# Kernel tuning notes

Measured on AMD Instinct MI355X. Metric: run time of the kernel, lower is better.

The kernel has to match this reference:

```python
import jax, jax.numpy as jnp
import numpy as np

L_FREQ = 6            # positional-encoding frequencies -> enc dim 3 + 3*2*6 = 39
SKIP = 4              # skip-connection layer index
BMIN, BMAX = -1.0, 1.0
RESCALE = 1.0
SCALE_MLP = 1.0
SDF_THR = 5e-5
ITERS_MAX = 8
RES = 128             # opt.Res (MAX_SAMPLES)
B, R = 1, 8192
N = B * R
PICK = 4096


def embed(xyz):
    # rescale into the AABB then NeRF positional encoding; (..., 3) -> (..., 39)
    xn = ((xyz - BMIN) / (BMAX - BMIN) * 2.0 - 1.0) * RESCALE
    freqs = (2.0 ** jnp.arange(L_FREQ)).astype(xyz.dtype)
    ang = xn[..., None, :] * freqs[:, None]                # (..., L, 3)
    flat = ang.reshape(*ang.shape[:-2], -1)                # (..., 3*L)
    return jnp.concatenate([xn, jnp.sin(flat), jnp.cos(flat)], axis=-1)


def mlp(enc, ws, bs):
    # VolSDF Geometry MLP: softplus(beta=100) activations, skip concat at layer SKIP
    h = enc
    for i in range(len(ws)):
        if i == SKIP:
            h = jnp.concatenate([h, enc], axis=-1)
        h = h @ ws[i] + bs[i]
        if i < len(ws) - 1:
            h = jax.nn.softplus(100.0 * h) / 100.0
    return h


def infer_sdf(xyz, ws, bs):
    # opt.data.inside == True, bg_sdf == False branch
    return mlp(embed(xyz), ws, bs)[..., 0] / SCALE_MLP


def ray_aabb(o, d):
    # slab test (RayAABBIntersector): entry/exit distances, near clamped to 0
    inv = 1.0 / d
    t1 = (BMIN - o) * inv
    t2 = (BMAX - o) * inv
    tmin = jnp.max(jnp.minimum(t1, t2), axis=-1)
    tmax = jnp.min(jnp.maximum(t1, t2), axis=-1)
    return jnp.maximum(tmin, 0.0), tmax


def sphere_trace(o, d, ws, bs):
    # o, d: (N, 3). Runs exactly ITERS_MAX masked iterations (the torch loop only
    # breaks early when ALL rays converge; masked rays add curr_sdf==0 so the
    # per-ray math is identical).
    tmin, tmax = ray_aabb(o, d)
    p_s = o + tmin[:, None] * d
    next_s = infer_sdf(p_s, ws, bs)
    next_e = infer_sdf(o + tmax[:, None] * d, ws, bs)
    mask_s = jnp.ones((o.shape[0],), bool)
    mask_e = jnp.ones((o.shape[0],), bool)

    def step(carry, _):
        acc_s, acc_e, next_s, next_e, mask_s, mask_e, p_s = carry
        curr_s = jnp.where(jnp.abs(next_s) <= SDF_THR, 0.0, next_s)
        curr_e = jnp.where(jnp.abs(next_e) <= SDF_THR, 0.0, next_e)
        mask_s = mask_s & (jnp.abs(curr_s) > SDF_THR)
        mask_e = mask_e & (jnp.abs(curr_e) > SDF_THR)
        track_pt = p_s                                  # appended BEFORE the march
        acc_s = jnp.minimum(acc_s + curr_s, tmax)
        acc_e = jnp.minimum(acc_e + curr_e, tmax)
        p_s = o + acc_s[:, None] * d
        p_e = o + acc_e[:, None] * d
        next_s = jnp.where(mask_s, infer_sdf(p_s, ws, bs), next_s)
        next_e = jnp.where(mask_e, infer_sdf(p_e, ws, bs), next_e)
        ok = acc_s < acc_e
        return (acc_s, acc_e, next_s, next_e, mask_s & ok, mask_e & ok, p_s), track_pt

    carry0 = (tmin, tmax, next_s, next_e, mask_s, mask_e, p_s)
    carry, track = jax.lax.scan(step, carry0, None, length=ITERS_MAX)
    acc_e = carry[1]
    pts_tracks = jnp.transpose(track, (1, 0, 2))        # (N, T, 3)
    return pts_tracks, acc_e, tmin, tmax


def setup_inputs() -> dict:
    key = jax.random.key(0)
    ks = jax.random.split(key, 16)
    u = jax.random.normal(ks[0], (B, R, 3), jnp.float32)
    u = u / jnp.linalg.norm(u, axis=-1, keepdims=True)
    ray0 = 3.0 * u                                       # origins on radius-3 sphere
    tgt = 0.3 * jax.random.normal(ks[1], (B, R, 3), jnp.float32)
    rd = tgt - ray0
    ray_direction = rd / jnp.linalg.norm(rd, axis=-1, keepdims=True)
    factor_rand = jax.random.uniform(ks[2], (B, R), jnp.float32)
    pick_ind = jax.random.permutation(ks[3], N)[:PICK].astype(jnp.int32)
    dims_in = [39, 256, 256, 256, 295, 256, 256, 256, 256]
    dims_out = [256] * 8 + [257]
    inp = {"ray0": ray0, "ray_direction": ray_direction,
           "factor_rand": factor_rand, "pick_ind": pick_ind}
    for i in range(9):
        inp[f"w{i}"] = jax.random.normal(ks[4 + (i % 12)], (dims_in[i], dims_out[i]),
                                           jnp.float32) / np.sqrt(dims_in[i]).astype(np.float32)
        inp[f"b{i}"] = jnp.zeros((dims_out[i],), jnp.float32)
    return inp


def reference(ray0, ray_direction, factor_rand, pick_ind,
              w0, b0, w1, b1, w2, b2, w3, b3, w4, b4, w5, b5, w6, b6, w7, b7, w8, b8):
    ws = [w0, w1, w2, w3, w4, w5, w6, w7, w8]
    bs = [b0, b1, b2, b3, b4, b5, b6, b7, b8]
    o = ray0.reshape(-1, 3)
    d = ray_direction.reshape(-1, 3)
    pts_tracks, acc_e, min_dis, max_dis = sphere_trace(o, d, ws, bs)
    sdf_tracks = infer_sdf(pts_tracks, ws, bs)          # (N, T)
    sdf_sum = jnp.sum(sdf_tracks, axis=-1)              # (N,)
    shp = ray0.shape[:-1]
    d_pred = jnp.minimum((sdf_sum + min_dis).reshape(shp), max_dis.reshape(shp))
    finish_mask = jnp.abs(sdf_tracks[:, -1]) < (BMAX - BMIN) / 10.0 / RES
    d_up = jnp.minimum(1.5 * acc_e.reshape(shp), max_dis.reshape(shp))
    d_sample = (1.0 - factor_rand) * d_up + factor_rand * min_dis.reshape(shp)
    sampled = ray0 + d_sample[..., None] * ray_direction
    sampled_pts = jnp.concatenate([pts_tracks[pick_ind].reshape(1, -1, 3),
                                   sampled.reshape(1, -1, 3)], axis=1)
    return d_pred, sdf_tracks[:, -1], sampled_pts, finish_mask
```

## Files before the change

### kernel.cpp

```cpp
#include <hip/hip_runtime.h>
#include <math.h>

#define NR 8192
#define NPICK 4096
#define SDF_THR_C 5e-5f

#define OUT_DPRED 0
#define OUT_SDFL  8192
#define OUT_SAMP  16384
#define OUT_FIN   139264

typedef __attribute__((ext_vector_type(8))) short short8v;
typedef __attribute__((ext_vector_type(4))) float f32x4;

#define SK  320
#define SKB 640

struct Wptrs { const float* w[8]; };
struct EvalP {
  const float* b[8];
  const float* b8;
  const unsigned short* WTi;
  const float* w8c;
};

__device__ __forceinline__ unsigned short f2bf(float f) {
  unsigned int u = __float_as_uint(f);
  unsigned int r = u + 0x7FFFu + ((u >> 16) & 1u);
  return (unsigned short)(r >> 16);
}
__device__ __forceinline__ float bf2f(unsigned short h) {
  return __uint_as_float(((unsigned int)h) << 16);
}
__device__ __forceinline__ float softplus100(float h) {
  float z = 100.0f * h;
  return (fmaxf(z, 0.0f) + __logf(1.0f + __expf(-fabsf(z)))) * 0.01f;
}

__global__ void prep_transpose(Wptrs wp, unsigned short* __restrict__ WTi)
{
  __shared__ unsigned short sh[64 * 66];
  __shared__ unsigned short sl[64 * 66];
  const int Kreal[8] = {39,256,256,256,295,256,256,256};
  const int Kp[8]    = {64,256,256,256,320,256,256,256};
  const int WB[8]    = {0,16384,81920,147456,212992,294912,360448,425984};
  const int cum[9]   = {0,4,20,36,52,72,88,104,120};
  int b = blockIdx.x;
  int l = 0;
  while (l < 7 && b >= cum[l + 1]) ++l;
  int tile = b - cum[l];
  int tk_n = Kp[l] >> 6;
  int tk = tile % tk_n, tc = tile / tk_n;
  const float* __restrict__ W = wp.w[l];
  int t = threadIdx.x;
  #pragma unroll
  for (int i = 0; i < 16; ++i) {
    int id = t + i * 256;
    int kl = id >> 6, cl = id & 63;
    int k = tk * 64 + kl, c = tc * 64 + cl;
    float v = (k < Kreal[l]) ? W[k * 256 + c] : 0.0f;
    unsigned short h = f2bf(v);
    unsigned short lo = f2bf(v - bf2f(h));
    sh[kl * 66 + cl] = h;
    sl[kl * 66 + cl] = lo;
  }
  __syncthreads();
  const int nksL = Kp[l] >> 5;
  #pragma unroll
  for (int i = 0; i < 16; ++i) {
    int id = t + i * 256;
    int cl = id >> 6, kl = id & 63;
    int col = tc * 64 + cl;
    int k = tk * 64 + kl;
    int g = col >> 4, lr = col & 15;
    int ksg = k >> 5, lq = (k >> 3) & 3, e = k & 7;
    int lane = lq * 16 + lr;
    size_t base = 2 * (size_t)WB[l] + ((size_t)(g * nksL + ksg)) * 1024 + lane * 8 + e;
    WTi[base]       = sh[kl * 66 + cl];
    WTi[base + 512] = sl[kl * 66 + cl];
  }
}

__global__ void prep_w8(const float* __restrict__ w8, float* __restrict__ w8c)
{
  int t = threadIdx.x;
  w8c[t] = w8[(size_t)t * 257];
}

template<int NKS, int KPL>
__device__ __forceinline__ void layer_bpre(
    const unsigned short* __restrict__ wt, const float* __restrict__ bias,
    unsigned short* Ah, unsigned short* Al,
    int lq, int lr, int cw, int swA)
{
  const char* ahc = (const char*)Ah;
  const char* alc = (const char*)Al;
  f32x4 acc[4];
  #pragma unroll
  for (int i = 0; i < 4; ++i) acc[i] = (f32x4){0.f, 0.f, 0.f, 0.f};

  const int col = cw + lr;
  const unsigned short* wcol = wt + (size_t)(cw >> 4) * NKS * 1024 + (lq * 16 + lr) * 8;

  short8v Bh[2], Bl[2];
  Bh[0] = *(const short8v*)(wcol);
  Bl[0] = *(const short8v*)(wcol + 512);

  #pragma unroll
  for (int ks = 0; ks < NKS; ++ks) {
    const int cur = ks & 1, nxt = cur ^ 1;
    if (ks + 1 < NKS) {
      const unsigned short* wn = wcol + (size_t)(ks + 1) * 1024;
      Bh[nxt] = *(const short8v*)(wn);
      Bl[nxt] = *(const short8v*)(wn + 512);
    }
    int ax = (ks * 64 + lq * 16) ^ swA;
    short8v ah[4], al[4];
    #pragma unroll
    for (int rt = 0; rt < 4; ++rt) {
      ah[rt] = *(const short8v*)(ahc + (rt * 16 + lr) * SKB + ax);
      al[rt] = *(const short8v*)(alc + (rt * 16 + lr) * SKB + ax);
    }
    #pragma unroll
    for (int rt = 0; rt < 4; ++rt) {
      acc[rt] = __builtin_amdgcn_mfma_f32_16x16x32_bf16(ah[rt], Bh[cur], acc[rt], 0, 0, 0);
      acc[rt] = __builtin_amdgcn_mfma_f32_16x16x32_bf16(al[rt], Bh[cur], acc[rt], 0, 0, 0);
      acc[rt] = __builtin_amdgcn_mfma_f32_16x16x32_bf16(ah[rt], Bl[cur], acc[rt], 0, 0, 0);
    }
  }

  __syncthreads();

  char* ahw = (char*)Ah;
  char* alw = (char*)Al;
  {
    float bv = bias[col];
    int cb2 = col * 2;
    #pragma unroll
    for (int rt = 0; rt < 4; ++rt) {
      #pragma unroll
      for (int r = 0; r < 4; ++r) {
        float h = softplus100(acc[rt][r] + bv);
        unsigned short hh = f2bf(h);
        unsigned short hl = f2bf(h - bf2f(hh));
        int row = rt * 16 + lq * 4 + r;
        int addr = row * SKB + (cb2 ^ ((row & 7) << 4));
        *(unsigned short*)(ahw + addr) = hh;
        *(unsigned short*)(alw + addr) = hl;
      }
    }
  }
  __syncthreads();
}

__global__ __launch_bounds__(1024, 1)
void eval_mfma(const float* __restrict__ pts, float* __restrict__ sdf_out, EvalP P)
{
  __shared__ __align__(16) unsigned short Ah[64 * SK];
  __shared__ __align__(16) unsigned short Al[64 * SK];
  __shared__ float enc[64 * 40];
  __shared__ float red[8 * 64];
  const int WBA[8] = {0,16384,81920,147456,212992,294912,360448,425984};

  const int t = threadIdx.x;
  const int rbase = blockIdx.x * 64;

  if (t < 64) {
    const int r = rbase + t;
    float x = pts[3*r+0], y = pts[3*r+1], z = pts[3*r+2];
    float xn = ((x + 1.0f) * 0.5f) * 2.0f - 1.0f;
    float yn = ((y + 1.0f) * 0.5f) * 2.0f - 1.0f;
    float zn = ((z + 1.0f) * 0.5f) * 2.0f - 1.0f;
    float* row = enc + t * 40;
    row[0] = xn; row[1] = yn; row[2] = zn;
    float f = 1.0f;
    for (int lf = 0; lf < 6; ++lf) {
      float ax = xn * f, ay = yn * f, az = zn * f;
      row[3  + lf*3 + 0] = sinf(ax);
      row[3  + lf*3 + 1] = sinf(ay);
      row[3  + lf*3 + 2] = sinf(az);
      row[21 + lf*3 + 0] = cosf(ax);
      row[21 + lf*3 + 1] = cosf(ay);
      row[21 + lf*3 + 2] = cosf(az);
      f *= 2.0f;
    }
  }
  __syncthreads();

  {
    char* ahp = (char*)Ah;
    char* alp = (char*)Al;
    int row = t >> 4, c4 = t & 15;
    int sw = (row & 7) << 4;
    #pragma unroll
    for (int reg = 0; reg < 2; ++reg) {
      int koff = reg ? 256 : 0;
      #pragma unroll
      for (int e = 0; e < 4; e += 2) {
        int kl = c4 * 4 + e;
        float v0 = (kl     < 39) ? enc[row * 40 + kl]     : 0.0f;
        float v1 = (kl + 1 < 39) ? enc[row * 40 + kl + 1] : 0.0f;
        unsigned short h0 = f2bf(v0), h1 = f2bf(v1);
        unsigned short q0 = f2bf(v0 - bf2f(h0)), q1 = f2bf(v1 - bf2f(h1));
        int addr = row * SKB + (((koff + kl) * 2) ^ sw);
        *(unsigned int*)(ahp + addr) = (unsigned)h0 | ((unsigned)h1 << 16);
        *(unsigned int*)(alp + addr) = (unsigned)q0 | ((unsigned)q1 << 16);
      }
    }
  }
  __syncthreads();

  const int lane = t & 63, wv = t >> 6;
  const int lq = lane >> 4, lr = lane & 15;
  const int cw = wv * 16;
  const char* ahc = (const char*)Ah;
  const int swA = (lr & 7) << 4;

  layer_bpre<2, 64>(P.WTi + 2 * (size_t)WBA[0], P.b[0], Ah, Al, lq, lr, cw, swA);
  #pragma unroll 1
  for (int l = 1; l < 8; ++l) {
    if (l == 4)
      layer_bpre<10, 320>(P.WTi + 2 * (size_t)WBA[4], P.b[4], Ah, Al, lq, lr, cw, swA);
    else
      layer_bpre<8, 256>(P.WTi + 2 * (size_t)WBA[l], P.b[l], Ah, Al, lq, lr, cw, swA);
  }

  {
    const char* alc = (const char*)Al;
    if (t < 512) {
      int row = t & 63, part = t >> 6;
      int sw = (row & 7) << 4;
      float s = 0.0f;
      #pragma unroll
      for (int c = 0; c < 4; ++c) {
        int k = part * 32 + c * 8;
        int addr = row * SKB + ((k * 2) ^ sw);
        short8v vh = *(const short8v*)(ahc + addr);
        short8v vl = *(const short8v*)(alc + addr);
        #pragma unroll
        for (int e = 0; e < 8; ++e) {
          float h = bf2f((unsigned short)vh[e]) + bf2f((unsigned short)vl[e]);
          s = fmaf(h, P.w8c[k + e], s);
        }
      }
      red[part * 64 + row] = s;
    }
    __syncthreads();
    if (t < 64) {
      float tot = P.b8[0];
      #pragma unroll
      for (int p = 0; p < 8; ++p) tot += red[p * 64 + t];
      sdf_out[rbase + t] = tot;
    }
  }
}

__global__ void init_kernel(const float* __restrict__ ray0, const float* __restrict__ rdir,
                            float* tminA, float* tmaxA, float* evalpts, float* ptrack)
{
  int r = blockIdx.x * 256 + threadIdx.x;
  if (r >= NR) return;
  float ox = ray0[3*r], oy = ray0[3*r+1], oz = ray0[3*r+2];
  float dx = rdir[3*r], dy = rdir[3*r+1], dz = rdir[3*r+2];
  float ix = 1.0f/dx, iy = 1.0f/dy, iz = 1.0f/dz;
  float t1x = (-1.0f - ox)*ix, t2x = (1.0f - ox)*ix;
  float t1y = (-1.0f - oy)*iy, t2y = (1.0f - oy)*iy;
  float t1z = (-1.0f - oz)*iz, t2z = (1.0f - oz)*iz;
  float tmn = fmaxf(fmaxf(fminf(t1x,t2x), fminf(t1y,t2y)), fminf(t1z,t2z));
  float tmx = fminf(fminf(fmaxf(t1x,t2x), fmaxf(t1y,t2y)), fmaxf(t1z,t2z));
  tmn = fmaxf(tmn, 0.0f);
  tminA[r] = tmn; tmaxA[r] = tmx;
  float px = ox + tmn*dx, py = oy + tmn*dy, pz = oz + tmn*dz;
  float qx = ox + tmx*dx, qy = oy + tmx*dy, qz = oz + tmx*dz;
  evalpts[3*r+0] = px; evalpts[3*r+1] = py; evalpts[3*r+2] = pz;
  evalpts[3*(NR+r)+0] = qx; evalpts[3*(NR+r)+1] = qy; evalpts[3*(NR+r)+2] = qz;
  ptrack[r*24+0] = px; ptrack[r*24+1] = py; ptrack[r*24+2] = pz;
}

__global__ void march_kernel(const float* __restrict__ ray0, const float* __restrict__ rdir,
                             const float* __restrict__ raw,
                             float* next_s, float* next_e,
                             int* msel_s, int* msel_e, int* mcar_s, int* mcar_e,
                             float* accS, float* accE,
                             const float* __restrict__ tminA, const float* __restrict__ tmaxA,
                             float* strack, float* ptrack, float* evalpts, int tstep)
{
  int r = blockIdx.x * 256 + threadIdx.x;
  if (r >= NR) return;
  float tmn = tminA[r], tmx = tmaxA[r];
  float rs = raw[r], re = raw[NR + r];
  float ns, ne, as_, ae; int ms, me;
  if (tstep == 0) {
    ns = rs; ne = re; ms = 1; me = 1; as_ = tmn; ae = tmx;
    strack[r*8 + 0] = rs;
  } else {
    ns = next_s[r]; ne = next_e[r];
    ns = msel_s[r] ? rs : ns;
    ne = msel_e[r] ? re : ne;
    strack[r*8 + tstep] = rs;
    ms = mcar_s[r]; me = mcar_e[r];
    as_ = accS[r]; ae = accE[r];
  }
  float cs = (fabsf(ns) <= SDF_THR_C) ? 0.0f : ns;
  float ce = (fabsf(ne) <= SDF_THR_C) ? 0.0f : ne;
  ms = ms & ((fabsf(cs) > SDF_THR_C) ? 1 : 0);
  me = me & ((fabsf(ce) > SDF_THR_C) ? 1 : 0);
  as_ = fminf(as_ + cs, tmx);
  ae  = fminf(ae + ce, tmx);
  if (tstep < 7) {
    float ox = ray0[3*r], oy = ray0[3*r+1], oz = ray0[3*r+2];
    float dx = rdir[3*r], dy = rdir[3*r+1], dz = rdir[3*r+2];
    float px = ox + as_*dx, py = oy + as_*dy, pz = oz + as_*dz;
    float qx = ox + ae*dx,  qy = oy + ae*dy,  qz = oz + ae*dz;
    ptrack[r*24 + (tstep+1)*3 + 0] = px;
    ptrack[r*24 + (tstep+1)*3 + 1] = py;
    ptrack[r*24 + (tstep+1)*3 + 2] = pz;
    evalpts[3*r+0] = px; evalpts[3*r+1] = py; evalpts[3*r+2] = pz;
    evalpts[3*(NR+r)+0] = qx; evalpts[3*(NR+r)+1] = qy; evalpts[3*(NR+r)+2] = qz;
  }
  int ok = (as_ < ae) ? 1 : 0;
  msel_s[r] = ms;       msel_e[r] = me;
  mcar_s[r] = ms & ok;  mcar_e[r] = me & ok;
  next_s[r] = ns; next_e[r] = ne;
  accS[r] = as_; accE[r] = ae;
}

__global__ void finalize_kernel(const float* __restrict__ ray0, const float* __restrict__ rdir,
                                const float* __restrict__ frand, const int* __restrict__ pick,
                                const float* __restrict__ strack, const float* __restrict__ ptrack,
                                const float* __restrict__ accE,
                                const float* __restrict__ tminA, const float* __restrict__ tmaxA,
                                float* __restrict__ out)
{
  int r = blockIdx.x * 256 + threadIdx.x;
  if (r < NR) {
    float tmn = tminA[r], tmx = tmaxA[r];
    float sum = 0.f;
    #pragma unroll
    for (int tt = 0; tt < 8; ++tt) sum += strack[r*8 + tt];
    out[OUT_DPRED + r] = fminf(sum + tmn, tmx);
    float last = strack[r*8 + 7];
    out[OUT_SDFL + r] = last;
    out[OUT_FIN + r] = (fabsf(last) < 0.0015625f) ? 1.0f : 0.0f;
    float du = fminf(1.5f * accE[r], tmx);
    float fr = frand[r];
    float dsm = (1.0f - fr) * du + fr * tmn;
    float ox = ray0[3*r], oy = ray0[3*r+1], oz = ray0[3*r+2];
    float dx = rdir[3*r], dy = rdir[3*r+1], dz = rdir[3*r+2];
    int o2 = OUT_SAMP + 98304 + 3*r;
    out[o2+0] = ox + dsm*dx;
    out[o2+1] = oy + dsm*dy;
    out[o2+2] = oz + dsm*dz;
  }
  if (r < NPICK) {
    int ray = pick[r];
    #pragma unroll
    for (int i = 0; i < 24; ++i)
      out[OUT_SAMP + r*24 + i] = ptrack[ray*24 + i];
  }
}

extern "C" void kernel_launch(void* const* d_in, const int* in_sizes, int n_in,
                              void* d_out, int out_size, void* d_ws, size_t ws_size,
                              hipStream_t stream)
{
  const float* ray0  = (const float*)d_in[0];
  const float* rdir  = (const float*)d_in[1];
  const float* frand = (const float*)d_in[2];
  const int*   pick  = (const int*)d_in[3];
  Wptrs wp;
  EvalP ep;
  for (int i = 0; i < 8; ++i) {
    wp.w[i] = (const float*)d_in[4 + 2*i];
    ep.b[i] = (const float*)d_in[5 + 2*i];
  }
  const float* w8 = (const float*)d_in[20];
  ep.b8 = (const float*)d_in[21];

  float* ws = (float*)d_ws;
  float* evalpts = ws;
  float* raw     = evalpts + 49152;
  float* tminA   = raw + 16384;
  float* tmaxA   = tminA + 8192;
  float* nextS   = tmaxA + 8192;
  float* nextE   = nextS + 8192;
  float* accS    = nextE + 8192;
  float* accE    = accS + 8192;
  float* strack  = accE + 8192;
  float* ptrack  = strack + 65536;
  int*   mselS   = (int*)(ptrack + 196608);
  int*   mselE   = mselS + 8192;
  int*   mcarS   = mselE + 8192;
  int*   mcarE   = mcarS + 8192;
  float* w8c     = (float*)(mcarE + 8192);
  unsigned short* WTi = (unsigned short*)(w8c + 256);
  ep.WTi = WTi; ep.w8c = w8c;
  float* out = (float*)d_out;

  prep_transpose<<<120, 256, 0, stream>>>(wp, WTi);
  prep_w8<<<1, 256, 0, stream>>>(w8, w8c);
  init_kernel<<<NR/256, 256, 0, stream>>>(ray0, rdir, tminA, tmaxA, evalpts, ptrack);
  eval_mfma<<<(2*NR)/64, 1024, 0, stream>>>(evalpts, raw, ep);
  for (int t = 0; t < 8; ++t) {
    march_kernel<<<NR/256, 256, 0, stream>>>(ray0, rdir, raw, nextS, nextE,
                                             mselS, mselE, mcarS, mcarE,
                                             accS, accE, tminA, tmaxA,
                                             strack, ptrack, evalpts, t);
    if (t < 7)
      eval_mfma<<<(2*NR)/64, 1024, 0, stream>>>(evalpts, raw, ep);
  }
  finalize_kernel<<<NR/256, 256, 0, stream>>>(ray0, rdir, frand, pick,
                                              strack, ptrack, accE, tminA, tmaxA, out);
}
```

Before: 583.6 us.

## Fuse march step into MLP eval kernel, pairing start/end points per block

Each eval block now handles 32 rays, with their start and end points forming its 64 rows. After the MLP it runs the sphere-march update for those rays directly from shared memory, which removes the separate march kernel launches and the raw SDF global round-trip. The positional-encoding sin/cos setup is also spread across all threads instead of 64. The launch count is roughly halved, and the per-ray state update only occupies 32 threads at the tail of a 1024-thread block.

```diff
diff --git a/kernel.cpp b/kernel.cpp
--- a/kernel.cpp
+++ b/kernel.cpp
@@ -22,6 +22,12 @@
   const float* b8;
   const unsigned short* WTi;
   const float* w8c;
+  const float* ray0; const float* rdir;
+  float* tminA; float* tmaxA;
+  float* nextS; float* nextE;
+  int* mselS; int* mselE; int* mcarS; int* mcarE;
+  float* accS; float* accE;
+  float* strack; float* ptrack; float* evalpts;
 };
 
 __device__ __forceinline__ unsigned short f2bf(float f) {
@@ -154,36 +160,31 @@
 }
 
 __global__ __launch_bounds__(1024, 1)
-void eval_mfma(const float* __restrict__ pts, float* __restrict__ sdf_out, EvalP P)
+void eval_fused(EvalP P, int tstep)
 {
   __shared__ __align__(16) unsigned short Ah[64 * SK];
   __shared__ __align__(16) unsigned short Al[64 * SK];
   __shared__ float enc[64 * 40];
   __shared__ float red[8 * 64];
+  __shared__ float sdfv[64];
   const int WBA[8] = {0,16384,81920,147456,212992,294912,360448,425984};
 
   const int t = threadIdx.x;
-  const int rbase = blockIdx.x * 64;
-
-  if (t < 64) {
-    const int r = rbase + t;
-    float x = pts[3*r+0], y = pts[3*r+1], z = pts[3*r+2];
-    float xn = ((x + 1.0f) * 0.5f) * 2.0f - 1.0f;
-    float yn = ((y + 1.0f) * 0.5f) * 2.0f - 1.0f;
-    float zn = ((z + 1.0f) * 0.5f) * 2.0f - 1.0f;
-    float* row = enc + t * 40;
-    row[0] = xn; row[1] = yn; row[2] = zn;
-    float f = 1.0f;
-    for (int lf = 0; lf < 6; ++lf) {
-      float ax = xn * f, ay = yn * f, az = zn * f;
-      row[3  + lf*3 + 0] = sinf(ax);
-      row[3  + lf*3 + 1] = sinf(ay);
-      row[3  + lf*3 + 2] = sinf(az);
-      row[21 + lf*3 + 0] = cosf(ax);
-      row[21 + lf*3 + 1] = cosf(ay);
-      row[21 + lf*3 + 2] = cosf(az);
-      f *= 2.0f;
-    }
+  const int rayb = blockIdx.x * 32;
+
+  if (t < 192) {
+    int row = t / 3, c = t - row * 3;
+    int idx = (row < 32) ? (rayb + row) : (NR + rayb + row - 32);
+    float p = P.evalpts[3 * idx + c];
+    enc[row * 40 + c] = ((p + 1.0f) * 0.5f) * 2.0f - 1.0f;
+  }
+  __syncthreads();
+  for (int i = t; i < 64 * 36; i += 1024) {
+    int row = i / 36, j = i - row * 36;
+    int jj = (j < 18) ? j : j - 18;
+    int c = jj % 3, lf = jj / 3;
+    float arg = enc[row * 40 + c] * (float)(1 << lf);
+    enc[row * 40 + 3 + j] = (j < 18) ? sinf(arg) : cosf(arg);
   }
   __syncthreads();
 
@@ -250,8 +251,48 @@
       float tot = P.b8[0];
       #pragma unroll
       for (int p = 0; p < 8; ++p) tot += red[p * 64 + t];
-      sdf_out[rbase + t] = tot;
-    }
+      sdfv[t] = tot;
+    }
+    __syncthreads();
+  }
+
+  if (t < 32) {
+    int r = rayb + t;
+    float tmn = P.tminA[r], tmx = P.tmaxA[r];
+    float rs = sdfv[t], re = sdfv[32 + t];
+    float ns, ne, as_, ae; int ms, me;
+    if (tstep == 0) {
+      ns = rs; ne = re; ms = 1; me = 1; as_ = tmn; ae = tmx;
+    } else {
+      ns = P.nextS[r]; ne = P.nextE[r];
+      ns = P.mselS[r] ? rs : ns;
+      ne = P.mselE[r] ? re : ne;
+      ms = P.mcarS[r]; me = P.mcarE[r];
+      as_ = P.accS[r]; ae = P.accE[r];
+    }
+    P.strack[r*8 + tstep] = rs;
+    float cs = (fabsf(ns) <= SDF_THR_C) ? 0.0f : ns;
+    float ce = (fabsf(ne) <= SDF_THR_C) ? 0.0f : ne;
+    ms = ms & ((fabsf(cs) > SDF_THR_C) ? 1 : 0);
+    me = me & ((fabsf(ce) > SDF_THR_C) ? 1 : 0);
+    as_ = fminf(as_ + cs, tmx);
+    ae  = fminf(ae + ce, tmx);
+    if (tstep < 7) {
+      float ox = P.ray0[3*r], oy = P.ray0[3*r+1], oz = P.ray0[3*r+2];
+      float dx = P.rdir[3*r], dy = P.rdir[3*r+1], dz = P.rdir[3*r+2];
+      float px = ox + as_*dx, py = oy + as_*dy, pz = oz + as_*dz;
+      float qx = ox + ae*dx,  qy = oy + ae*dy,  qz = oz + ae*dz;
+      P.ptrack[r*24 + (tstep+1)*3 + 0] = px;
+      P.ptrack[r*24 + (tstep+1)*3 + 1] = py;
+      P.ptrack[r*24 + (tstep+1)*3 + 2] = pz;
+      P.evalpts[3*r+0] = px; P.evalpts[3*r+1] = py; P.evalpts[3*r+2] = pz;
+      P.evalpts[3*(NR+r)+0] = qx; P.evalpts[3*(NR+r)+1] = qy; P.evalpts[3*(NR+r)+2] = qz;
+    }
+    int ok = (as_ < ae) ? 1 : 0;
+    P.mselS[r] = ms;       P.mselE[r] = me;
+    P.mcarS[r] = ms & ok;  P.mcarE[r] = me & ok;
+    P.nextS[r] = ns; P.nextE[r] = ne;
+    P.accS[r] = as_; P.accE[r] = ae;
   }
 }
 
@@ -277,54 +318,6 @@
   ptrack[r*24+0] = px; ptrack[r*24+1] = py; ptrack[r*24+2] = pz;
 }
 
-__global__ void march_kernel(const float* __restrict__ ray0, const float* __restrict__ rdir,
-                             const float* __restrict__ raw,
-                             float* next_s, float* next_e,
-                             int* msel_s, int* msel_e, int* mcar_s, int* mcar_e,
-                             float* accS, float* accE,
-                             const float* __restrict__ tminA, const float* __restrict__ tmaxA,
-                             float* strack, float* ptrack, float* evalpts, int tstep)
-{
-  int r = blockIdx.x * 256 + threadIdx.x;
-  if (r >= NR) return;
-  float tmn = tminA[r], tmx = tmaxA[r];
-  float rs = raw[r], re = raw[NR + r];
-  float ns, ne, as_, ae; int ms, me;
-  if (tstep == 0) {
-    ns = rs; ne = re; ms = 1; me = 1; as_ = tmn; ae = tmx;
-    strack[r*8 + 0] = rs;
-  } else {
-    ns = next_s[r]; ne = next_e[r];
-    ns = msel_s[r] ? rs : ns;
-    ne = msel_e[r] ? re : ne;
-    strack[r*8 + tstep] = rs;
-    ms = mcar_s[r]; me = mcar_e[r];
-    as_ = accS[r]; ae = accE[r];
-  }
-  float cs = (fabsf(ns) <= SDF_THR_C) ? 0.0f : ns;
-  float ce = (fabsf(ne) <= SDF_THR_C) ? 0.0f : ne;
-  ms = ms & ((fabsf(cs) > SDF_THR_C) ? 1 : 0);
-  me = me & ((fabsf(ce) > SDF_THR_C) ? 1 : 0);
-  as_ = fminf(as_ + cs, tmx);
-  ae  = fminf(ae + ce, tmx);
-  if (tstep < 7) {
-    float ox = ray0[3*r], oy = ray0[3*r+1], oz = ray0[3*r+2];
-    float dx = rdir[3*r], dy = rdir[3*r+1], dz = rdir[3*r+2];
-    float px = ox + as_*dx, py = oy + as_*dy, pz = oz + as_*dz;
-    float qx = ox + ae*dx,  qy = oy + ae*dy,  qz = oz + ae*dz;
-    ptrack[r*24 + (tstep+1)*3 + 0] = px;
-    ptrack[r*24 + (tstep+1)*3 + 1] = py;
-    ptrack[r*24 + (tstep+1)*3 + 2] = pz;
-    evalpts[3*r+0] = px; evalpts[3*r+1] = py; evalpts[3*r+2] = pz;
-    evalpts[3*(NR+r)+0] = qx; evalpts[3*(NR+r)+1] = qy; evalpts[3*(NR+r)+2] = qz;
-  }
-  int ok = (as_ < ae) ? 1 : 0;
-  msel_s[r] = ms;       msel_e[r] = me;
-  mcar_s[r] = ms & ok;  mcar_e[r] = me & ok;
-  next_s[r] = ns; next_e[r] = ne;
-  accS[r] = as_; accE[r] = ae;
-}
-
 __global__ void finalize_kernel(const float* __restrict__ ray0, const float* __restrict__ rdir,
                                 const float* __restrict__ frand, const int* __restrict__ pick,
                                 const float* __restrict__ strack, const float* __restrict__ ptrack,
@@ -376,11 +369,11 @@
   }
   const float* w8 = (const float*)d_in[20];
   ep.b8 = (const float*)d_in[21];
+  ep.ray0 = ray0; ep.rdir = rdir;
 
   float* ws = (float*)d_ws;
   float* evalpts = ws;
-  float* raw     = evalpts + 49152;
-  float* tminA   = raw + 16384;
+  float* tminA   = evalpts + 49152;
   float* tmaxA   = tminA + 8192;
   float* nextS   = tmaxA + 8192;
   float* nextE   = nextS + 8192;
@@ -395,20 +388,18 @@
   float* w8c     = (float*)(mcarE + 8192);
   unsigned short* WTi = (unsigned short*)(w8c + 256);
   ep.WTi = WTi; ep.w8c = w8c;
+  ep.tminA = tminA; ep.tmaxA = tmaxA;
+  ep.nextS = nextS; ep.nextE = nextE;
+  ep.mselS = mselS; ep.mselE = mselE; ep.mcarS = mcarS; ep.mcarE = mcarE;
+  ep.accS = accS; ep.accE = accE;
+  ep.strack = strack; ep.ptrack = ptrack; ep.evalpts = evalpts;
   float* out = (float*)d_out;
 
   prep_transpose<<<120, 256, 0, stream>>>(wp, WTi);
   prep_w8<<<1, 256, 0, stream>>>(w8, w8c);
   init_kernel<<<NR/256, 256, 0, stream>>>(ray0, rdir, tminA, tmaxA, evalpts, ptrack);
-  eval_mfma<<<(2*NR)/64, 1024, 0, stream>>>(evalpts, raw, ep);
-  for (int t = 0; t < 8; ++t) {
-    march_kernel<<<NR/256, 256, 0, stream>>>(ray0, rdir, raw, nextS, nextE,
-                                             mselS, mselE, mcarS, mcarE,
-                                             accS, accE, tminA, tmaxA,
-                                             strack, ptrack, evalpts, t);
-    if (t < 7)
-      eval_mfma<<<(2*NR)/64, 1024, 0, stream>>>(evalpts, raw, ep);
-  }
+  for (int t = 0; t < 8; ++t)
+    eval_fused<<<NR/32, 1024, 0, stream>>>(ep, t);
   finalize_kernel<<<NR/256, 256, 0, stream>>>(ray0, rdir, frand, pick,
                                               strack, ptrack, accE, tminA, tmaxA, out);
 }
```

Measured after the change: 542.9 us. -7.0%, faster.
